# Optimization experiments

Measured on AMD Instinct MI355X. Metric: run time of the kernel, lower is better.

The kernel has to match this reference:

```python
import jax, jax.numpy as jnp
import numpy as np

B, S, IN, H, C = 4, 1024, 1024, 256, 8

def setup_inputs() -> dict:
    key = jax.random.key(0)
    ks = jax.random.split(key, 9)
    scale_in = 1.0 / np.sqrt(IN)
    scale_h2 = 1.0 / np.sqrt(2 * H)
    return {
        "seq_feats": jax.random.normal(ks[0], (B, S, IN), dtype=jnp.float32),
        "U": jax.random.normal(ks[1], (H, C, H), dtype=jnp.float32) * 0.02,
        "W_weight": jax.random.uniform(ks[2], (C, 2 * H), minval=-scale_h2, maxval=scale_h2, dtype=jnp.float32),
        "W_bias": jax.random.uniform(ks[3], (C,), minval=-scale_h2, maxval=scale_h2, dtype=jnp.float32),
        "start_w": jax.random.uniform(ks[4], (H, IN), minval=-scale_in, maxval=scale_in, dtype=jnp.float32),
        "start_b": jax.random.uniform(ks[5], (H,), minval=-scale_in, maxval=scale_in, dtype=jnp.float32),
        "end_w": jax.random.uniform(ks[6], (H, IN), minval=-scale_in, maxval=scale_in, dtype=jnp.float32),
        "end_b": jax.random.uniform(ks[7], (H,), minval=-scale_in, maxval=scale_in, dtype=jnp.float32),
    }

def reference(seq_feats, U, W_weight, W_bias, start_w, start_b, end_w, end_b):
    # Hs, He: [b, s, h]
    Hs = jnp.einsum('bsi,hi->bsh', seq_feats, start_w) + start_b
    He = jnp.einsum('bsi,hi->bsh', seq_feats, end_w) + end_b
    # biaffine: [b, s, e, c]
    biaff = jnp.einsum('bsh,hcg,beg->bsec', Hs, U, He)
    # Linear over concat([Hs_repeat, He_repeat]) == split-weight broadcast sum
    Ws, We = W_weight[:, :256], W_weight[:, 256:]
    lin = (jnp.einsum('bsh,ch->bsc', Hs, Ws)[:, :, None, :]
           + jnp.einsum('beh,ch->bec', He, We)[:, None, :, :]
           + W_bias)
    return biaff + lin
```

## Files before the change

kernel.cpp:

```cpp
#include <hip/hip_runtime.h>
#include <stdint.h>


#define BDIM 256

typedef float f32x4 __attribute__((ext_vector_type(4)));
typedef __bf16 bf16x8 __attribute__((ext_vector_type(8)));
typedef unsigned int u32;
typedef const __attribute__((address_space(1))) u32* gas_ptr;
typedef __attribute__((address_space(3))) u32* las_ptr;

static __device__ __forceinline__ void load_lds16(const void* g, void* l) {
  __builtin_amdgcn_global_load_lds((gas_ptr)g, (las_ptr)l, 16, 0, 0);
}

static __device__ __forceinline__ unsigned short f32_to_bf16(float f) {
  union { float f; u32 u; } v; v.f = f;
  u32 r = v.u + 0x7FFFu + ((v.u >> 16) & 1u);
  return (unsigned short)(r >> 16);
}
static __device__ __forceinline__ float bf16lo_to_f32(u32 u) {
  union { u32 u; float f; } v; v.u = u << 16;
  return v.f;
}
static __device__ __forceinline__ float bf16hi_to_f32(u32 u) {
  union { u32 u; float f; } v; v.u = u & 0xFFFF0000u;
  return v.f;
}

template <int IM, int EPI>
__global__ __launch_bounds__(BDIM, 2)
void gemm_bt(const unsigned short* __restrict__ Aall,
             const unsigned short* __restrict__ Ball,
             void* __restrict__ OutAll,
             const int N, const int K, const int lda, const int ldb,
             const long long strideA, const long long strideB, const long long strideO,
             const float* __restrict__ bias0,
             const float* __restrict__ bias1,
             const float* __restrict__ linSall,
             const float* __restrict__ linEall)
{
  constexpr int WM = IM * 16;
  constexpr int TM = 2 * WM;

  __shared__ unsigned short lsA[TM * 32];
  __shared__ unsigned short lsB[128 * 32];

  const int tid  = threadIdx.x;
  const int lane = tid & 63;
  const int wv   = tid >> 6;
  const int wr   = wv >> 1;
  const int wc   = wv & 1;
  const int z    = blockIdx.z;

  const int gx = gridDim.x;
  const int nwg = gx * gridDim.y;
  int id = blockIdx.y * gx + blockIdx.x;
  {
    const int q = nwg >> 3;
    id = (id & 7) * q + (id >> 3);
  }
  const int n0 = (id % gx) * 128;
  const int m0 = (id / gx) * TM;

  const unsigned short* A  = Aall + (size_t)z * strideA;
  const unsigned short* Bm = Ball + (size_t)z * strideB;

  f32x4 acc[IM][4];
#pragma unroll
  for (int i = 0; i < IM; ++i)
#pragma unroll
    for (int j = 0; j < 4; ++j) acc[i][j] = (f32x4)0.f;

  const int rA = lane & 15;
  const int ko = (lane >> 4) * 8;

  for (int kt = 0; kt < K; kt += 32) {
    constexpr int CA = TM * 4;
#pragma unroll
    for (int it = 0; it < CA / BDIM; ++it) {
      const int chunk = it * BDIM + tid;
      const int row = chunk >> 2;
      const int ce = (chunk & 3) * 8;
      load_lds16(A + (size_t)(m0 + row) * lda + (kt + ce), &lsA[chunk * 8]);
    }
#pragma unroll
    for (int it = 0; it < 2; ++it) {
      const int chunk = it * BDIM + tid;
      const int row = chunk >> 2;
      const int ce = (chunk & 3) * 8;
      load_lds16(Bm + (size_t)(n0 + row) * ldb + (kt + ce), &lsB[chunk * 8]);
    }
    __syncthreads();

    bf16x8 aF[IM], bF[4];
#pragma unroll
    for (int i = 0; i < IM; ++i)
      aF[i] = *reinterpret_cast<const bf16x8*>(&lsA[(wr * WM + i * 16 + rA) * 32 + ko]);
#pragma unroll
    for (int j = 0; j < 4; ++j)
      bF[j] = *reinterpret_cast<const bf16x8*>(&lsB[(wc * 64 + j * 16 + rA) * 32 + ko]);
#pragma unroll
    for (int i = 0; i < IM; ++i)
#pragma unroll
      for (int j = 0; j < 4; ++j)
        acc[i][j] = __builtin_amdgcn_mfma_f32_16x16x32_bf16(aF[i], bF[j], acc[i][j], 0, 0, 0);
    __syncthreads();
  }

  const int rgr = (lane >> 4) * 4;

  if constexpr (EPI == 2) {
    float* Out = (float*)OutAll + (size_t)z * strideO;
    const float* lS = linSall + (size_t)z * 8192;
    const float* lE = linEall + (size_t)z * 8192;
#pragma unroll
    for (int i = 0; i < IM; ++i) {
#pragma unroll
      for (int j = 0; j < 4; ++j) {
        const int mBase = m0 + wr * WM + i * 16 + rgr;
        const int e = n0 + wc * 64 + j * 16 + rA;
        const int s = mBase >> 3;
        const int c0 = mBase & 7;
        const float4 ls4 = *reinterpret_cast<const float4*>(lS + mBase);
        const float4 le4 = *reinterpret_cast<const float4*>(lE + (e << 3) + c0);
        float4 o;
        o.x = acc[i][j][0] + ls4.x + le4.x;
        o.y = acc[i][j][1] + ls4.y + le4.y;
        o.z = acc[i][j][2] + ls4.z + le4.z;
        o.w = acc[i][j][3] + ls4.w + le4.w;
        *reinterpret_cast<float4*>(Out + ((size_t)s << 13) + ((size_t)e << 3) + c0) = o;
      }
    }
  } else {
    unsigned short* Out = (unsigned short*)OutAll;
#pragma unroll
    for (int i = 0; i < IM; ++i) {
#pragma unroll
      for (int j = 0; j < 4; ++j) {
        const int mBase = m0 + wr * WM + i * 16 + rgr;
        const int n = n0 + wc * 64 + j * 16 + rA;
        float bn = 0.f;
        if constexpr (EPI == 1) bn = (n < 256) ? bias0[n] : bias1[n - 256];
#pragma unroll
        for (int r = 0; r < 4; ++r) {
          Out[(size_t)(mBase + r) * N + n] = f32_to_bf16(acc[i][j][r] + bn);
        }
      }
    }
  }
}

__global__ void prep_kernel(const float* __restrict__ seq,
                            const float* __restrict__ sw,
                            const float* __restrict__ ew,
                            const float* __restrict__ U,
                            unsigned short* __restrict__ Xbf,
                            unsigned short* __restrict__ wbf,
                            unsigned short* __restrict__ Ut)
{
  const int bid = blockIdx.x;
  const int tid = threadIdx.x;
  if (bid < 4096) {
    const int i = bid * 1024 + tid * 4;
    const float4 v = *reinterpret_cast<const float4*>(seq + i);
    ushort4 o;
    o.x = f32_to_bf16(v.x); o.y = f32_to_bf16(v.y);
    o.z = f32_to_bf16(v.z); o.w = f32_to_bf16(v.w);
    *reinterpret_cast<ushort4*>(Xbf + i) = o;
  } else if (bid < 4608) {
    const int i = (bid - 4096) * 1024 + tid * 4;
    const float* src = (i < 262144) ? (sw + i) : (ew + (i - 262144));
    const float4 v = *reinterpret_cast<const float4*>(src);
    ushort4 o;
    o.x = f32_to_bf16(v.x); o.y = f32_to_bf16(v.y);
    o.z = f32_to_bf16(v.z); o.w = f32_to_bf16(v.w);
    *reinterpret_cast<ushort4*>(wbf + i) = o;
  } else {
    const int i = (bid - 4608) * 1024 + tid * 4;
    const int n = i >> 8;
    const int h = i & 255;
    ushort4 o;
    o.x = f32_to_bf16(U[(size_t)(h + 0) * 2048 + n]);
    o.y = f32_to_bf16(U[(size_t)(h + 1) * 2048 + n]);
    o.z = f32_to_bf16(U[(size_t)(h + 2) * 2048 + n]);
    o.w = f32_to_bf16(U[(size_t)(h + 3) * 2048 + n]);
    *reinterpret_cast<ushort4*>(Ut + i) = o;
  }
}

__global__ void lin_kernel(const unsigned short* __restrict__ Hboth,
                           const float* __restrict__ Ww,
                           const float* __restrict__ Wb,
                           float* __restrict__ linS,
                           float* __restrict__ linE)
{
  const int idx = blockIdx.x * BDIM + threadIdx.x;
  if (idx >= 4096 * 8) return;
  const int m = idx >> 3;
  const int c = idx & 7;
  const uint4* hs4 = reinterpret_cast<const uint4*>(Hboth + (size_t)m * 512);
  const uint4* he4 = reinterpret_cast<const uint4*>(Hboth + (size_t)m * 512 + 256);
  const float* ws = Ww + c * 512;
  const float* we = ws + 256;
  float s1 = 0.f, s2 = 0.f;
#pragma unroll 4
  for (int t = 0; t < 32; ++t) {
    const uint4 a = hs4[t];
    const uint4 b = he4[t];
    const u32 aw[4] = {a.x, a.y, a.z, a.w};
    const u32 bw[4] = {b.x, b.y, b.z, b.w};
#pragma unroll
    for (int q = 0; q < 4; ++q) {
      const int h = t * 8 + q * 2;
      s1 += bf16lo_to_f32(aw[q]) * ws[h] + bf16hi_to_f32(aw[q]) * ws[h + 1];
      s2 += bf16lo_to_f32(bw[q]) * we[h] + bf16hi_to_f32(bw[q]) * we[h + 1];
    }
  }
  linS[idx] = s1;
  linE[idx] = s2 + Wb[c];
}

extern "C" void kernel_launch(void* const* d_in, const int* in_sizes, int n_in,
                              void* d_out, int out_size, void* d_ws, size_t ws_size,
                              hipStream_t stream)
{
  const float* seq = (const float*)d_in[0];
  const float* U   = (const float*)d_in[1];
  const float* Ww  = (const float*)d_in[2];
  const float* Wb  = (const float*)d_in[3];
  const float* sw  = (const float*)d_in[4];
  const float* sb  = (const float*)d_in[5];
  const float* ew  = (const float*)d_in[6];
  const float* eb  = (const float*)d_in[7];
  float* out = (float*)d_out;

  unsigned short* Xbf   = (unsigned short*)d_ws;
  unsigned short* wbf   = Xbf  + 4194304;
  unsigned short* Utbf  = wbf  + 524288;
  unsigned short* Hboth = Utbf + 524288;
  unsigned short* Tbf   = Hboth + 2097152;
  float* linS = (float*)(Tbf + 8388608);
  float* linE = linS + 32768;

  prep_kernel<<<5120, BDIM, 0, stream>>>(seq, sw, ew, U, Xbf, wbf, Utbf);

  gemm_bt<2, 1><<<dim3(4, 64, 1), BDIM, 0, stream>>>(
      Xbf, wbf, Hboth, 512, 1024, 1024, 1024, 0, 0, 0, sb, eb, nullptr, nullptr);

  lin_kernel<<<128, BDIM, 0, stream>>>(Hboth, Ww, Wb, linS, linE);

  gemm_bt<4, 0><<<dim3(16, 32, 1), BDIM, 0, stream>>>(
      Hboth, Utbf, Tbf, 2048, 256, 512, 256, 0, 0, 0,
      nullptr, nullptr, nullptr, nullptr);

  gemm_bt<4, 2><<<dim3(8, 64, 4), BDIM, 0, stream>>>(
      Tbf, Hboth + 256, out, 1024, 256, 256, 512,
      (long long)8192 * 256, (long long)1024 * 512, (long long)8388608,
      nullptr, nullptr, linS, linE);
}
```

Baseline: 98.47 us.

## Add dedicated 256x256 double-buffered pipelined kernel for the biaffine output GEMM

Replaces the generic 128-wide tile GEMM for the final biaffine stage with a specialised 512-thread kernel. It uses 256x256 output tiles, a K-step of 64, XOR-swizzled LDS staging and double buffering. Global-to-LDS loads are interleaved with MFMA quarters under explicit barriers and setprio, aiming to hide memory latency and raise reuse per tile on this output-write-bound stage. It needs 128KB of dynamic LDS per block and sets that attribute on every launch, and the larger register footprint may limit occupancy.

```diff
diff --git a/kernel.cpp b/kernel.cpp
--- a/kernel.cpp
+++ b/kernel.cpp
@@ -7,6 +7,7 @@
 typedef float f32x4 __attribute__((ext_vector_type(4)));
 typedef __bf16 bf16x8 __attribute__((ext_vector_type(8)));
 typedef unsigned int u32;
+typedef unsigned short u16;
 typedef const __attribute__((address_space(1))) u32* gas_ptr;
 typedef __attribute__((address_space(3))) u32* las_ptr;
 
@@ -14,10 +15,10 @@
   __builtin_amdgcn_global_load_lds((gas_ptr)g, (las_ptr)l, 16, 0, 0);
 }
 
-static __device__ __forceinline__ unsigned short f32_to_bf16(float f) {
+static __device__ __forceinline__ u16 f32_to_bf16(float f) {
   union { float f; u32 u; } v; v.f = f;
   u32 r = v.u + 0x7FFFu + ((v.u >> 16) & 1u);
-  return (unsigned short)(r >> 16);
+  return (u16)(r >> 16);
 }
 static __device__ __forceinline__ float bf16lo_to_f32(u32 u) {
   union { u32 u; float f; } v; v.u = u << 16;
@@ -28,30 +29,204 @@
   return v.f;
 }
 
+#define K3_LDSA(b) ((b) * 32768)
+#define K3_LDSB(b) ((b) * 32768 + 16384)
+
+#define STG(dstofs, src, srow, ld, kt)                                         \
+  load_lds16((src) + (size_t)((srow) + (tid >> 3)) * (ld) + (kt) +             \
+                 (((tid & 7) ^ ((tid >> 3) & 7)) << 3),                        \
+             &lds[(dstofs) + tid * 8])
+
+#define STG_A(b, mh, t) do {                                                   \
+    STG(K3_LDSA(b) + (mh) * 4096,       Ag, m0 + (mh) * 64,       256, (t)*64);\
+    STG(K3_LDSA(b) + ((mh)+2) * 4096,   Ag, m0 + 128 + (mh) * 64, 256, (t)*64);\
+  } while (0)
+
+#define STG_B(b, h, t) do {                                                    \
+    STG(K3_LDSB(b) + (2*(h)) * 4096,    Bgz, n0 + (h) * 128,      512, (t)*64);\
+    STG(K3_LDSB(b) + (2*(h)+1) * 4096,  Bgz, n0 + (h) * 128 + 64, 512, (t)*64);\
+  } while (0)
+
+#define RD_A(b, mh)                                                            \
+  _Pragma("unroll")                                                            \
+  for (int mi = 0; mi < 4; ++mi) {                                             \
+    const int r = wr * 128 + (mh) * 64 + mi * 16 + rA;                         \
+    _Pragma("unroll")                                                          \
+    for (int ks = 0; ks < 2; ++ks)                                             \
+      aF[mi][ks] = *reinterpret_cast<const bf16x8*>(                           \
+          &lds[K3_LDSA(b) + r * 64 + ((((ks << 2) | kq) ^ (rA & 7)) << 3)]);   \
+  }
+
+#define RD_B(b)                                                                \
+  _Pragma("unroll")                                                            \
+  for (int nh = 0; nh < 2; ++nh)                                               \
+  _Pragma("unroll")                                                            \
+  for (int ni = 0; ni < 2; ++ni) {                                             \
+    const int r = wc * 64 + nh * 32 + ni * 16 + rA;                            \
+    _Pragma("unroll")                                                          \
+    for (int ks = 0; ks < 2; ++ks)                                             \
+      bF[nh][ni][ks] = *reinterpret_cast<const bf16x8*>(                       \
+          &lds[K3_LDSB(b) + r * 64 + ((((ks << 2) | kq) ^ (rA & 7)) << 3)]);   \
+  }
+
+#define MFMA_Q(mh, nh)                                                         \
+  __builtin_amdgcn_s_setprio(1);                                               \
+  _Pragma("unroll")                                                            \
+  for (int mi = 0; mi < 4; ++mi)                                               \
+  _Pragma("unroll")                                                            \
+  for (int ni = 0; ni < 2; ++ni)                                               \
+  _Pragma("unroll")                                                            \
+  for (int ks = 0; ks < 2; ++ks)                                               \
+    acc[(mh)*4 + mi][(nh)*2 + ni] = __builtin_amdgcn_mfma_f32_16x16x32_bf16(   \
+        aF[mi][ks], bF[nh][ni][ks], acc[(mh)*4 + mi][(nh)*2 + ni], 0, 0, 0);   \
+  __builtin_amdgcn_s_setprio(0);
+
+#define BARRIER_MID()                                                          \
+  __builtin_amdgcn_sched_barrier(0);                                           \
+  __builtin_amdgcn_s_barrier();                                                \
+  asm volatile("s_waitcnt lgkmcnt(0)" ::: "memory");                           \
+  __builtin_amdgcn_sched_barrier(0)
+
+#define BARRIER_END()                                                          \
+  __builtin_amdgcn_sched_barrier(0);                                           \
+  __builtin_amdgcn_s_barrier()
+
+__global__ __launch_bounds__(512, 2)
+void gemm256_biaff(const u16* __restrict__ Tall,
+                   const u16* __restrict__ Bg,
+                   float* __restrict__ Out,
+                   const float* __restrict__ linSall,
+                   const float* __restrict__ linEall)
+{
+  extern __shared__ u16 lds[];
+
+  const int tid  = threadIdx.x;
+  const int lane = tid & 63;
+  const int wv   = tid >> 6;
+  const int wr   = wv >> 2;
+  const int wc   = wv & 3;
+  const int rA   = lane & 15;
+  const int kq   = lane >> 4;
+  const int z    = blockIdx.z;
+
+  int id = blockIdx.y * gridDim.x + blockIdx.x;
+  id = (id & 7) * 16 + (id >> 3);
+  const int n0 = (id & 3) * 256;
+  const int m0 = (id >> 2) * 256;
+
+  const u16* Ag  = Tall + (size_t)z * (8192 * 256);
+  const u16* Bgz = Bg   + (size_t)z * (1024 * 512);
+
+  f32x4 acc[8][4];
+#pragma unroll
+  for (int i = 0; i < 8; ++i)
+#pragma unroll
+    for (int j = 0; j < 4; ++j) acc[i][j] = (f32x4)0.f;
+
+  bf16x8 aF[4][2];
+  bf16x8 bF[2][2][2];
+
+  STG_A(0, 0, 0); STG_A(0, 1, 0); STG_B(0, 0, 0); STG_B(0, 1, 0);
+  STG_A(1, 0, 1);
+  asm volatile("s_waitcnt vmcnt(2)" ::: "memory");
+  __builtin_amdgcn_s_barrier();
+
+  constexpr int NT = 4;
+#pragma unroll
+  for (int i = 0; i < NT / 2; ++i) {
+    const int t1 = 2 * i + 1, t2 = 2 * i + 2, t3 = 2 * i + 3;
+    RD_A(0, 0); RD_B(0);
+    STG_A(1, 1, t1);
+    BARRIER_MID();
+    MFMA_Q(0, 0);
+    BARRIER_END();
+    STG_B(1, 0, t1);
+    BARRIER_MID();
+    MFMA_Q(0, 1);
+    BARRIER_END();
+    RD_A(0, 1);
+    STG_B(1, 1, t1);
+    BARRIER_MID();
+    MFMA_Q(1, 1);
+    BARRIER_END();
+    if (t2 < NT) {
+      STG_A(0, 0, t2);
+      asm volatile("s_waitcnt vmcnt(2)" ::: "memory");
+    } else {
+      asm volatile("s_waitcnt vmcnt(0)" ::: "memory");
+    }
+    BARRIER_MID();
+    MFMA_Q(1, 0);
+    BARRIER_END();
+    RD_A(1, 0); RD_B(1);
+    if (t2 < NT) STG_A(0, 1, t2);
+    BARRIER_MID();
+    MFMA_Q(0, 0);
+    BARRIER_END();
+    if (t2 < NT) STG_B(0, 0, t2);
+    BARRIER_MID();
+    MFMA_Q(0, 1);
+    BARRIER_END();
+    RD_A(1, 1);
+    if (t2 < NT) STG_B(0, 1, t2);
+    BARRIER_MID();
+    MFMA_Q(1, 1);
+    BARRIER_END();
+    if (t3 < NT) {
+      STG_A(1, 0, t3);
+      asm volatile("s_waitcnt vmcnt(2)" ::: "memory");
+    } else {
+      asm volatile("s_waitcnt vmcnt(0)" ::: "memory");
+    }
+    BARRIER_MID();
+    MFMA_Q(1, 0);
+    BARRIER_END();
+  }
+
+  const int rgr = kq * 4;
+  float* OutZ = Out + (size_t)z * 8388608;
+  const float* lS = linSall + (size_t)z * 8192;
+  const float* lE = linEall + (size_t)z * 8192;
+#pragma unroll
+  for (int mf = 0; mf < 8; ++mf) {
+#pragma unroll
+    for (int nf = 0; nf < 4; ++nf) {
+      const int mBase = m0 + wr * 128 + mf * 16 + rgr;
+      const int e = n0 + wc * 64 + (nf >> 1) * 32 + (nf & 1) * 16 + rA;
+      const int s = mBase >> 3;
+      const int c0 = mBase & 7;
+      const float4 ls4 = *reinterpret_cast<const float4*>(lS + mBase);
+      const float4 le4 = *reinterpret_cast<const float4*>(lE + (e << 3) + c0);
+      float4 o;
+      o.x = acc[mf][nf][0] + ls4.x + le4.x;
+      o.y = acc[mf][nf][1] + ls4.y + le4.y;
+      o.z = acc[mf][nf][2] + ls4.z + le4.z;
+      o.w = acc[mf][nf][3] + ls4.w + le4.w;
+      *reinterpret_cast<float4*>(OutZ + ((size_t)s << 13) + ((size_t)e << 3) + c0) = o;
+    }
+  }
+}
+
 template <int IM, int EPI>
 __global__ __launch_bounds__(BDIM, 2)
-void gemm_bt(const unsigned short* __restrict__ Aall,
-             const unsigned short* __restrict__ Ball,
+void gemm_bt(const u16* __restrict__ Aall,
+             const u16* __restrict__ Ball,
              void* __restrict__ OutAll,
              const int N, const int K, const int lda, const int ldb,
-             const long long strideA, const long long strideB, const long long strideO,
              const float* __restrict__ bias0,
-             const float* __restrict__ bias1,
-             const float* __restrict__ linSall,
-             const float* __restrict__ linEall)
+             const float* __restrict__ bias1)
 {
   constexpr int WM = IM * 16;
   constexpr int TM = 2 * WM;
 
-  __shared__ unsigned short lsA[TM * 32];
-  __shared__ unsigned short lsB[128 * 32];
+  __shared__ u16 lsA[TM * 32];
+  __shared__ u16 lsB[128 * 32];
 
   const int tid  = threadIdx.x;
   const int lane = tid & 63;
   const int wv   = tid >> 6;
   const int wr   = wv >> 1;
   const int wc   = wv & 1;
-  const int z    = blockIdx.z;
 
   const int gx = gridDim.x;
   const int nwg = gx * gridDim.y;
@@ -63,8 +238,8 @@
   const int n0 = (id % gx) * 128;
   const int m0 = (id / gx) * TM;
 
-  const unsigned short* A  = Aall + (size_t)z * strideA;
-  const unsigned short* Bm = Ball + (size_t)z * strideB;
+  const u16* A  = Aall;
+  const u16* Bm = Ball;
 
   f32x4 acc[IM][4];
 #pragma unroll
@@ -109,43 +284,18 @@
   }
 
   const int rgr = (lane >> 4) * 4;
-
-  if constexpr (EPI == 2) {
-    float* Out = (float*)OutAll + (size_t)z * strideO;
-    const float* lS = linSall + (size_t)z * 8192;
-    const float* lE = linEall + (size_t)z * 8192;
-#pragma unroll
-    for (int i = 0; i < IM; ++i) {
-#pragma unroll
-      for (int j = 0; j < 4; ++j) {
-        const int mBase = m0 + wr * WM + i * 16 + rgr;
-        const int e = n0 + wc * 64 + j * 16 + rA;
-        const int s = mBase >> 3;
-        const int c0 = mBase & 7;
-        const float4 ls4 = *reinterpret_cast<const float4*>(lS + mBase);
-        const float4 le4 = *reinterpret_cast<const float4*>(lE + (e << 3) + c0);
-        float4 o;
-        o.x = acc[i][j][0] + ls4.x + le4.x;
-        o.y = acc[i][j][1] + ls4.y + le4.y;
-        o.z = acc[i][j][2] + ls4.z + le4.z;
-        o.w = acc[i][j][3] + ls4.w + le4.w;
-        *reinterpret_cast<float4*>(Out + ((size_t)s << 13) + ((size_t)e << 3) + c0) = o;
-      }
-    }
-  } else {
-    unsigned short* Out = (unsigned short*)OutAll;
-#pragma unroll
-    for (int i = 0; i < IM; ++i) {
-#pragma unroll
-      for (int j = 0; j < 4; ++j) {
-        const int mBase = m0 + wr * WM + i * 16 + rgr;
-        const int n = n0 + wc * 64 + j * 16 + rA;
-        float bn = 0.f;
-        if constexpr (EPI == 1) bn = (n < 256) ? bias0[n] : bias1[n - 256];
-#pragma unroll
-        for (int r = 0; r < 4; ++r) {
-          Out[(size_t)(mBase + r) * N + n] = f32_to_bf16(acc[i][j][r] + bn);
-        }
+  u16* Out = (u16*)OutAll;
+#pragma unroll
+  for (int i = 0; i < IM; ++i) {
+#pragma unroll
+    for (int j = 0; j < 4; ++j) {
+      const int mBase = m0 + wr * WM + i * 16 + rgr;
+      const int n = n0 + wc * 64 + j * 16 + rA;
+      float bn = 0.f;
+      if constexpr (EPI == 1) bn = (n < 256) ? bias0[n] : bias1[n - 256];
+#pragma unroll
+      for (int r = 0; r < 4; ++r) {
+        Out[(size_t)(mBase + r) * N + n] = f32_to_bf16(acc[i][j][r] + bn);
       }
     }
   }
@@ -155,9 +305,9 @@
                             const float* __restrict__ sw,
                             const float* __restrict__ ew,
                             const float* __restrict__ U,
-                            unsigned short* __restrict__ Xbf,
-                            unsigned short* __restrict__ wbf,
-                            unsigned short* __restrict__ Ut)
+                            u16* __restrict__ Xbf,
+                            u16* __restrict__ wbf,
+                            u16* __restrict__ Ut)
 {
   const int bid = blockIdx.x;
   const int tid = threadIdx.x;
@@ -189,7 +339,7 @@
   }
 }
 
-__global__ void lin_kernel(const unsigned short* __restrict__ Hboth,
+__global__ void lin_kernel(const u16* __restrict__ Hboth,
                            const float* __restrict__ Ww,
                            const float* __restrict__ Wb,
                            float* __restrict__ linS,
@@ -235,27 +385,26 @@
   const float* eb  = (const float*)d_in[7];
   float* out = (float*)d_out;
 
-  unsigned short* Xbf   = (unsigned short*)d_ws;
-  unsigned short* wbf   = Xbf  + 4194304;
-  unsigned short* Utbf  = wbf  + 524288;
-  unsigned short* Hboth = Utbf + 524288;
-  unsigned short* Tbf   = Hboth + 2097152;
+  u16* Xbf   = (u16*)d_ws;
+  u16* wbf   = Xbf  + 4194304;
+  u16* Utbf  = wbf  + 524288;
+  u16* Hboth = Utbf + 524288;
+  u16* Tbf   = Hboth + 2097152;
   float* linS = (float*)(Tbf + 8388608);
   float* linE = linS + 32768;
 
   prep_kernel<<<5120, BDIM, 0, stream>>>(seq, sw, ew, U, Xbf, wbf, Utbf);
 
   gemm_bt<2, 1><<<dim3(4, 64, 1), BDIM, 0, stream>>>(
-      Xbf, wbf, Hboth, 512, 1024, 1024, 1024, 0, 0, 0, sb, eb, nullptr, nullptr);
+      Xbf, wbf, Hboth, 512, 1024, 1024, 1024, sb, eb);
 
   lin_kernel<<<128, BDIM, 0, stream>>>(Hboth, Ww, Wb, linS, linE);
 
   gemm_bt<4, 0><<<dim3(16, 32, 1), BDIM, 0, stream>>>(
-      Hboth, Utbf, Tbf, 2048, 256, 512, 256, 0, 0, 0,
-      nullptr, nullptr, nullptr, nullptr);
-
-  gemm_bt<4, 2><<<dim3(8, 64, 4), BDIM, 0, stream>>>(
-      Tbf, Hboth + 256, out, 1024, 256, 256, 512,
-      (long long)8192 * 256, (long long)1024 * 512, (long long)8388608,
-      nullptr, nullptr, linS, linE);
-}
+      Hboth, Utbf, Tbf, 2048, 256, 512, 256, nullptr, nullptr);
+
+  hipFuncSetAttribute(reinterpret_cast<const void*>(&gemm256_biaff),
+                      hipFuncAttributeMaxDynamicSharedMemorySize, 131072);
+  gemm256_biaff<<<dim3(4, 32, 4), 512, 131072, stream>>>(
+      Tbf, Hboth + 256, out, linS, linE);
+}
```

Result: no change. 97.33 us (-1.2%).

## Specialize biaffine GEMM with K=64 swizzled LDS tiles and merge lin into T GEMM

Applied to the files above, without the earlier changes.

Adds a dedicated kernel for the final biaffine GEMM. It stages 64-wide K tiles into LDS with an XOR swizzle, which halves the number of barrier iterations and reduces LDS bank conflicts, and it requests occupancy 4. The lin_kernel is folded into the T=Hs·U GEMM launch as extra blocks, removing one kernel launch and letting the small lin work overlap with the GEMM. The generic gemm_bt loses its batched and EPI==2 paths. The larger LDS footprint and higher occupancy target may raise register pressure.

```diff
diff --git a/kernel.cpp b/kernel.cpp
--- a/kernel.cpp
+++ b/kernel.cpp
@@ -7,6 +7,7 @@
 typedef float f32x4 __attribute__((ext_vector_type(4)));
 typedef __bf16 bf16x8 __attribute__((ext_vector_type(8)));
 typedef unsigned int u32;
+typedef unsigned short u16;
 typedef const __attribute__((address_space(1))) u32* gas_ptr;
 typedef __attribute__((address_space(3))) u32* las_ptr;
 
@@ -14,10 +15,10 @@
   __builtin_amdgcn_global_load_lds((gas_ptr)g, (las_ptr)l, 16, 0, 0);
 }
 
-static __device__ __forceinline__ unsigned short f32_to_bf16(float f) {
+static __device__ __forceinline__ u16 f32_to_bf16(float f) {
   union { float f; u32 u; } v; v.f = f;
   u32 r = v.u + 0x7FFFu + ((v.u >> 16) & 1u);
-  return (unsigned short)(r >> 16);
+  return (u16)(r >> 16);
 }
 static __device__ __forceinline__ float bf16lo_to_f32(u32 u) {
   union { u32 u; float f; } v; v.u = u << 16;
@@ -28,30 +29,125 @@
   return v.f;
 }
 
-template <int IM, int EPI>
-__global__ __launch_bounds__(BDIM, 2)
-void gemm_bt(const unsigned short* __restrict__ Aall,
-             const unsigned short* __restrict__ Ball,
-             void* __restrict__ OutAll,
-             const int N, const int K, const int lda, const int ldb,
-             const long long strideA, const long long strideB, const long long strideO,
-             const float* __restrict__ bias0,
-             const float* __restrict__ bias1,
-             const float* __restrict__ linSall,
-             const float* __restrict__ linEall)
-{
-  constexpr int WM = IM * 16;
-  constexpr int TM = 2 * WM;
-
-  __shared__ unsigned short lsA[TM * 32];
-  __shared__ unsigned short lsB[128 * 32];
+static __device__ __forceinline__ void stage32(u16* lds, int dst, const u16* src,
+                                               int srow, int ld, int kcol, int tid) {
+  const int r = tid >> 3;
+  const int sl = tid & 7;
+  load_lds16(src + (size_t)(srow + r) * ld + kcol + ((sl ^ (r & 7)) << 3),
+             &lds[dst + tid * 8]);
+}
+
+static __device__ __forceinline__ bf16x8 rd64(const u16* lds, int base, int row, int kslot) {
+  return *reinterpret_cast<const bf16x8*>(&lds[base + row * 64 + ((kslot ^ (row & 7)) << 3)]);
+}
+
+__global__ __launch_bounds__(BDIM, 4)
+void gemm128_biaff(const u16* __restrict__ Tall,
+                   const u16* __restrict__ Bg,
+                   float* __restrict__ Out,
+                   const float* __restrict__ linSall,
+                   const float* __restrict__ linEall)
+{
+  __shared__ u16 lds[2 * 8192];
 
   const int tid  = threadIdx.x;
   const int lane = tid & 63;
   const int wv   = tid >> 6;
   const int wr   = wv >> 1;
   const int wc   = wv & 1;
+  const int rA   = lane & 15;
+  const int kq   = lane >> 4;
   const int z    = blockIdx.z;
+
+  int id = blockIdx.y * gridDim.x + blockIdx.x;
+  id = (id & 7) * 64 + (id >> 3);
+  const int n0 = (id & 7) * 128;
+  const int m0 = (id >> 3) * 128;
+
+  const u16* Ag  = Tall + (size_t)z * (8192 * 256);
+  const u16* Bgz = Bg   + (size_t)z * (1024 * 512);
+
+  f32x4 acc[4][4];
+#pragma unroll
+  for (int i = 0; i < 4; ++i)
+#pragma unroll
+    for (int j = 0; j < 4; ++j) acc[i][j] = (f32x4)0.f;
+
+#pragma unroll 1
+  for (int kt = 0; kt < 256; kt += 64) {
+#pragma unroll
+    for (int h = 0; h < 4; ++h)
+      stage32(lds, h * 2048, Ag, m0 + h * 32, 256, kt, tid);
+#pragma unroll
+    for (int h = 0; h < 4; ++h)
+      stage32(lds, 8192 + h * 2048, Bgz, n0 + h * 32, 512, kt, tid);
+    __syncthreads();
+
+    bf16x8 aF[4][2], bF[4][2];
+#pragma unroll
+    for (int mi = 0; mi < 4; ++mi)
+#pragma unroll
+      for (int ks = 0; ks < 2; ++ks)
+        aF[mi][ks] = rd64(lds, 0, wr * 64 + mi * 16 + rA, (ks << 2) | kq);
+#pragma unroll
+    for (int ni = 0; ni < 4; ++ni)
+#pragma unroll
+      for (int ks = 0; ks < 2; ++ks)
+        bF[ni][ks] = rd64(lds, 8192, wc * 64 + ni * 16 + rA, (ks << 2) | kq);
+#pragma unroll
+    for (int mi = 0; mi < 4; ++mi)
+#pragma unroll
+      for (int ni = 0; ni < 4; ++ni)
+#pragma unroll
+        for (int ks = 0; ks < 2; ++ks)
+          acc[mi][ni] = __builtin_amdgcn_mfma_f32_16x16x32_bf16(
+              aF[mi][ks], bF[ni][ks], acc[mi][ni], 0, 0, 0);
+    __syncthreads();
+  }
+
+  float* OutZ = Out + (size_t)z * 8388608;
+  const float* lS = linSall + (size_t)z * 8192;
+  const float* lE = linEall + (size_t)z * 8192;
+#pragma unroll
+  for (int mi = 0; mi < 4; ++mi) {
+#pragma unroll
+    for (int ni = 0; ni < 4; ++ni) {
+      const int mBase = m0 + wr * 64 + mi * 16 + kq * 4;
+      const int e = n0 + wc * 64 + ni * 16 + rA;
+      const int s = mBase >> 3;
+      const int c0 = mBase & 7;
+      const float4 ls4 = *reinterpret_cast<const float4*>(lS + mBase);
+      const float4 le4 = *reinterpret_cast<const float4*>(lE + (e << 3) + c0);
+      float4 o;
+      o.x = acc[mi][ni][0] + ls4.x + le4.x;
+      o.y = acc[mi][ni][1] + ls4.y + le4.y;
+      o.z = acc[mi][ni][2] + ls4.z + le4.z;
+      o.w = acc[mi][ni][3] + ls4.w + le4.w;
+      *reinterpret_cast<float4*>(OutZ + ((size_t)s << 13) + ((size_t)e << 3) + c0) = o;
+    }
+  }
+}
+
+template <int IM, int EPI>
+__global__ __launch_bounds__(BDIM, 2)
+void gemm_bt(const u16* __restrict__ Aall,
+             const u16* __restrict__ Ball,
+             void* __restrict__ OutAll,
+             const int N, const int K, const int lda, const int ldb,
+             const float* __restrict__ bias0,
+             const float* __restrict__ bias1)
+{
+  constexpr int WM = IM * 16;
+  constexpr int TM = 2 * WM;
+
+  __shared__ u16 lsA[TM * 32];
+  __shared__ u16 lsB[128 * 32];
+
+  const int tid  = threadIdx.x;
+  const int lane = tid & 63;
+  const int wv   = tid >> 6;
+  const int wr   = wv >> 1;
+  const int wc   = wv & 1;
 
   const int gx = gridDim.x;
   const int nwg = gx * gridDim.y;
@@ -63,8 +159,8 @@
   const int n0 = (id % gx) * 128;
   const int m0 = (id / gx) * TM;
 
-  const unsigned short* A  = Aall + (size_t)z * strideA;
-  const unsigned short* Bm = Ball + (size_t)z * strideB;
+  const u16* A  = Aall;
+  const u16* Bm = Ball;
 
   f32x4 acc[IM][4];
 #pragma unroll
@@ -109,44 +205,119 @@
   }
 
   const int rgr = (lane >> 4) * 4;
-
-  if constexpr (EPI == 2) {
-    float* Out = (float*)OutAll + (size_t)z * strideO;
-    const float* lS = linSall + (size_t)z * 8192;
-    const float* lE = linEall + (size_t)z * 8192;
-#pragma unroll
-    for (int i = 0; i < IM; ++i) {
-#pragma unroll
-      for (int j = 0; j < 4; ++j) {
-        const int mBase = m0 + wr * WM + i * 16 + rgr;
-        const int e = n0 + wc * 64 + j * 16 + rA;
-        const int s = mBase >> 3;
-        const int c0 = mBase & 7;
-        const float4 ls4 = *reinterpret_cast<const float4*>(lS + mBase);
-        const float4 le4 = *reinterpret_cast<const float4*>(lE + (e << 3) + c0);
-        float4 o;
-        o.x = acc[i][j][0] + ls4.x + le4.x;
-        o.y = acc[i][j][1] + ls4.y + le4.y;
-        o.z = acc[i][j][2] + ls4.z + le4.z;
-        o.w = acc[i][j][3] + ls4.w + le4.w;
-        *reinterpret_cast<float4*>(Out + ((size_t)s << 13) + ((size_t)e << 3) + c0) = o;
+  u16* Out = (u16*)OutAll;
+#pragma unroll
+  for (int i = 0; i < IM; ++i) {
+#pragma unroll
+    for (int j = 0; j < 4; ++j) {
+      const int mBase = m0 + wr * WM + i * 16 + rgr;
+      const int n = n0 + wc * 64 + j * 16 + rA;
+      float bn = 0.f;
+      if constexpr (EPI == 1) bn = (n < 256) ? bias0[n] : bias1[n - 256];
+#pragma unroll
+      for (int r = 0; r < 4; ++r) {
+        Out[(size_t)(mBase + r) * N + n] = f32_to_bf16(acc[i][j][r] + bn);
       }
     }
-  } else {
-    unsigned short* Out = (unsigned short*)OutAll;
-#pragma unroll
-    for (int i = 0; i < IM; ++i) {
-#pragma unroll
-      for (int j = 0; j < 4; ++j) {
-        const int mBase = m0 + wr * WM + i * 16 + rgr;
-        const int n = n0 + wc * 64 + j * 16 + rA;
-        float bn = 0.f;
-        if constexpr (EPI == 1) bn = (n < 256) ? bias0[n] : bias1[n - 256];
-#pragma unroll
-        for (int r = 0; r < 4; ++r) {
-          Out[(size_t)(mBase + r) * N + n] = f32_to_bf16(acc[i][j][r] + bn);
-        }
+  }
+}
+
+__global__ __launch_bounds__(BDIM, 2)
+void k2lin(const u16* __restrict__ Hboth,
+           const u16* __restrict__ Utbf,
+           u16* __restrict__ Tbf,
+           const float* __restrict__ Ww,
+           const float* __restrict__ Wb,
+           float* __restrict__ linS,
+           float* __restrict__ linE)
+{
+  const int bid = blockIdx.x;
+  const int tid = threadIdx.x;
+
+  if (bid >= 512) {
+    const int idx = (bid - 512) * BDIM + tid;
+    const int m = idx >> 3;
+    const int c = idx & 7;
+    const uint4* hs4 = reinterpret_cast<const uint4*>(Hboth + (size_t)m * 512);
+    const uint4* he4 = reinterpret_cast<const uint4*>(Hboth + (size_t)m * 512 + 256);
+    const float* wsp = Ww + c * 512;
+    const float* wep = wsp + 256;
+    float s1 = 0.f, s2 = 0.f;
+#pragma unroll 4
+    for (int t = 0; t < 32; ++t) {
+      const uint4 a = hs4[t];
+      const uint4 b = he4[t];
+      const u32 aw[4] = {a.x, a.y, a.z, a.w};
+      const u32 bw[4] = {b.x, b.y, b.z, b.w};
+#pragma unroll
+      for (int q = 0; q < 4; ++q) {
+        const int h = t * 8 + q * 2;
+        s1 += bf16lo_to_f32(aw[q]) * wsp[h] + bf16hi_to_f32(aw[q]) * wsp[h + 1];
+        s2 += bf16lo_to_f32(bw[q]) * wep[h] + bf16hi_to_f32(bw[q]) * wep[h + 1];
       }
+    }
+    linS[idx] = s1;
+    linE[idx] = s2 + Wb[c];
+    return;
+  }
+
+  __shared__ u16 lsA[128 * 32];
+  __shared__ u16 lsB[128 * 32];
+
+  int id = bid;
+  id = (id & 7) * 64 + (id >> 3);
+  const int n0 = (id & 15) * 128;
+  const int m0 = (id >> 4) * 128;
+
+  const int lane = tid & 63;
+  const int wv   = tid >> 6;
+  const int wr   = wv >> 1;
+  const int wc   = wv & 1;
+  const int rA   = lane & 15;
+  const int ko   = (lane >> 4) * 8;
+
+  f32x4 acc[4][4];
+#pragma unroll
+  for (int i = 0; i < 4; ++i)
+#pragma unroll
+    for (int j = 0; j < 4; ++j) acc[i][j] = (f32x4)0.f;
+
+  for (int kt = 0; kt < 256; kt += 32) {
+#pragma unroll
+    for (int it = 0; it < 2; ++it) {
+      const int chunk = it * BDIM + tid;
+      const int row = chunk >> 2;
+      const int ce = (chunk & 3) * 8;
+      load_lds16(Hboth + (size_t)(m0 + row) * 512 + (kt + ce), &lsA[chunk * 8]);
+      load_lds16(Utbf + (size_t)(n0 + row) * 256 + (kt + ce), &lsB[chunk * 8]);
+    }
+    __syncthreads();
+
+    bf16x8 aF[4], bF[4];
+#pragma unroll
+    for (int i = 0; i < 4; ++i)
+      aF[i] = *reinterpret_cast<const bf16x8*>(&lsA[(wr * 64 + i * 16 + rA) * 32 + ko]);
+#pragma unroll
+    for (int j = 0; j < 4; ++j)
+      bF[j] = *reinterpret_cast<const bf16x8*>(&lsB[(wc * 64 + j * 16 + rA) * 32 + ko]);
+#pragma unroll
+    for (int i = 0; i < 4; ++i)
+#pragma unroll
+      for (int j = 0; j < 4; ++j)
+        acc[i][j] = __builtin_amdgcn_mfma_f32_16x16x32_bf16(aF[i], bF[j], acc[i][j], 0, 0, 0);
+    __syncthreads();
+  }
+
+  const int rgr = (lane >> 4) * 4;
+#pragma unroll
+  for (int i = 0; i < 4; ++i) {
+#pragma unroll
+    for (int j = 0; j < 4; ++j) {
+      const int mBase = m0 + wr * 64 + i * 16 + rgr;
+      const int n = n0 + wc * 64 + j * 16 + rA;
+#pragma unroll
+      for (int r = 0; r < 4; ++r)
+        Tbf[(size_t)(mBase + r) * 2048 + n] = f32_to_bf16(acc[i][j][r]);
     }
   }
 }
@@ -155,9 +326,9 @@
                             const float* __restrict__ sw,
                             const float* __restrict__ ew,
                             const float* __restrict__ U,
-                            unsigned short* __restrict__ Xbf,
-                            unsigned short* __restrict__ wbf,
-                            unsigned short* __restrict__ Ut)
+                            u16* __restrict__ Xbf,
+                            u16* __restrict__ wbf,
+                            u16* __restrict__ Ut)
 {
   const int bid = blockIdx.x;
   const int tid = threadIdx.x;
@@ -189,38 +360,6 @@
   }
 }
 
-__global__ void lin_kernel(const unsigned short* __restrict__ Hboth,
-                           const float* __restrict__ Ww,
-                           const float* __restrict__ Wb,
-                           float* __restrict__ linS,
-                           float* __restrict__ linE)
-{
-  const int idx = blockIdx.x * BDIM + threadIdx.x;
-  if (idx >= 4096 * 8) return;
-  const int m = idx >> 3;
-  const int c = idx & 7;
-  const uint4* hs4 = reinterpret_cast<const uint4*>(Hboth + (size_t)m * 512);
-  const uint4* he4 = reinterpret_cast<const uint4*>(Hboth + (size_t)m * 512 + 256);
-  const float* ws = Ww + c * 512;
-  const float* we = ws + 256;
-  float s1 = 0.f, s2 = 0.f;
-#pragma unroll 4
-  for (int t = 0; t < 32; ++t) {
-    const uint4 a = hs4[t];
-    const uint4 b = he4[t];
-    const u32 aw[4] = {a.x, a.y, a.z, a.w};
-    const u32 bw[4] = {b.x, b.y, b.z, b.w};
-#pragma unroll
-    for (int q = 0; q < 4; ++q) {
-      const int h = t * 8 + q * 2;
-      s1 += bf16lo_to_f32(aw[q]) * ws[h] + bf16hi_to_f32(aw[q]) * ws[h + 1];
-      s2 += bf16lo_to_f32(bw[q]) * we[h] + bf16hi_to_f32(bw[q]) * we[h + 1];
-    }
-  }
-  linS[idx] = s1;
-  linE[idx] = s2 + Wb[c];
-}
-
 extern "C" void kernel_launch(void* const* d_in, const int* in_sizes, int n_in,
                               void* d_out, int out_size, void* d_ws, size_t ws_size,
                               hipStream_t stream)
@@ -235,27 +374,21 @@
   const float* eb  = (const float*)d_in[7];
   float* out = (float*)d_out;
 
-  unsigned short* Xbf   = (unsigned short*)d_ws;
-  unsigned short* wbf   = Xbf  + 4194304;
-  unsigned short* Utbf  = wbf  + 524288;
-  unsigned short* Hboth = Utbf + 524288;
-  unsigned short* Tbf   = Hboth + 2097152;
+  u16* Xbf   = (u16*)d_ws;
+  u16* wbf   = Xbf  + 4194304;
+  u16* Utbf  = wbf  + 524288;
+  u16* Hboth = Utbf + 524288;
+  u16* Tbf   = Hboth + 2097152;
   float* linS = (float*)(Tbf + 8388608);
   float* linE = linS + 32768;
 
   prep_kernel<<<5120, BDIM, 0, stream>>>(seq, sw, ew, U, Xbf, wbf, Utbf);
 
   gemm_bt<2, 1><<<dim3(4, 64, 1), BDIM, 0, stream>>>(
-      Xbf, wbf, Hboth, 512, 1024, 1024, 1024, 0, 0, 0, sb, eb, nullptr, nullptr);
-
-  lin_kernel<<<128, BDIM, 0, stream>>>(Hboth, Ww, Wb, linS, linE);
-
-  gemm_bt<4, 0><<<dim3(16, 32, 1), BDIM, 0, stream>>>(
-      Hboth, Utbf, Tbf, 2048, 256, 512, 256, 0, 0, 0,
-      nullptr, nullptr, nullptr, nullptr);
-
-  gemm_bt<4, 2><<<dim3(8, 64, 4), BDIM, 0, stream>>>(
-      Tbf, Hboth + 256, out, 1024, 256, 256, 512,
-      (long long)8192 * 256, (long long)1024 * 512, (long long)8388608,
-      nullptr, nullptr, linS, linE);
-}
+      Xbf, wbf, Hboth, 512, 1024, 1024, 1024, sb, eb);
+
+  k2lin<<<640, BDIM, 0, stream>>>(Hboth, Utbf, Tbf, Ww, Wb, linS, linE);
+
+  gemm128_biaff<<<dim3(8, 64, 4), BDIM, 0, stream>>>(
+      Tbf, Hboth + 256, out, linS, linE);
+}
```

Result: faster. 90.30 us (-8.3%).
